# Optimization experiments

Hardware: AMD Instinct MI355X
Metric: run time of the kernel (lower is better)

Reference implementation:

```python
import jax, jax.numpy as jnp
import numpy as np

CH_N = 12
CH_N_CONST = 4
CH_E = 8
MAX_V = 100.0
DT = 1.0


def _build_graph(n_inputs, n_hid, n_actions):
    n_nodes = n_inputs + n_hid + n_actions + 1
    mid = np.arange(n_inputs, n_inputs + n_hid + n_actions)
    src = np.concatenate([
        np.repeat(np.arange(n_inputs), n_hid + n_actions),
        np.repeat(np.arange(n_inputs, n_inputs + n_hid), n_hid + n_actions),
        np.full(n_nodes - 1, n_nodes - 1),
    ])
    tgt = np.concatenate([
        np.tile(mid, n_inputs),
        np.tile(mid, n_hid),
        np.arange(n_nodes - 1),
    ])
    return src.astype(np.int32), tgt.astype(np.int32), n_nodes


def setup_inputs() -> dict:
    n_inputs, n_hid, n_actions, B = 64, 1024, 16, 2
    src, tgt, n_nodes = _build_graph(n_inputs, n_hid, n_actions)
    n_edges = src.shape[0]
    key = jax.random.key(0)
    ks = jax.random.split(key, 10)
    s = 0.05
    d_msg_in = 2 + 2 * CH_N + CH_E          # 34
    d_msg_out = 2 * (CH_N - CH_N_CONST) + CH_E  # 24
    d_upd_in = 3 * CH_N - 2 * CH_N_CONST    # 28
    return {
        "nodes": jax.random.normal(ks[0], (B, n_nodes, CH_N), jnp.float32) * s,
        "edges": jax.random.normal(ks[1], (B, n_edges, CH_E), jnp.float32) * s,
        "msg_w1": jax.random.normal(ks[2], (32, d_msg_in), jnp.float32) * s,
        "msg_b1": jax.random.normal(ks[3], (32,), jnp.float32) * s,
        "msg_w2": jax.random.normal(ks[4], (d_msg_out, 32), jnp.float32) * s,
        "msg_b2": jax.random.normal(ks[5], (d_msg_out,), jnp.float32) * s,
        "upd_w1": jax.random.normal(ks[6], (16, d_upd_in), jnp.float32) * s,
        "upd_b1": jax.random.normal(ks[7], (16,), jnp.float32) * s,
        "upd_w2": jax.random.normal(ks[8], (CH_N - CH_N_CONST, 16), jnp.float32) * s,
        "upd_b2": jax.random.normal(ks[9], (CH_N - CH_N_CONST,), jnp.float32) * s,
        "sources": jnp.asarray(src),
        "targets": jnp.asarray(tgt),
    }


def reference(nodes, edges, msg_w1, msg_b1, msg_w2, msg_b2,
              upd_w1, upd_b1, upd_w2, upd_b2, sources, targets):
    B, N, _ = nodes.shape
    E = edges.shape[1]
    d = CH_N - CH_N_CONST  # dynamic node channels = 8

    # degree features (float for concat)
    out_degs = jax.ops.segment_sum(jnp.ones((E,), nodes.dtype), sources, num_segments=N)
    in_degs = jax.ops.segment_sum(jnp.ones((E,), nodes.dtype), targets, num_segments=N)
    od = jnp.broadcast_to(out_degs[sources][None, :, None], (B, E, 1))
    idg = jnp.broadcast_to(in_degs[targets][None, :, None], (B, E, 1))

    # gather + message MLP: [B, E, 34] -> 32 -> 24
    m_x = jnp.concatenate([nodes[:, sources], nodes[:, targets], edges, od, idg], axis=2)
    h = jax.nn.relu(jnp.einsum('bef,hf->beh', m_x, msg_w1) + msg_b1)
    m = jnp.einsum('beh,oh->beo', h, msg_w2) + msg_b2
    m_a, m_b, m_ab = m[..., :d], m[..., d:2 * d], m[..., 2 * d:]

    # scatter-aggregate (mean)
    agg_a = jnp.zeros((B, N, d), m.dtype).at[:, sources].add(m_a)
    agg_b = jnp.zeros((B, N, d), m.dtype).at[:, targets].add(m_b)
    agg_a = agg_a / jnp.maximum(out_degs, 1.0)[None, :, None]
    agg_b = agg_b / jnp.maximum(in_degs, 1.0)[None, :, None]

    # update MLP: [B, N, 28] -> 16 -> 8
    u_x = jnp.concatenate([agg_a, agg_b, nodes], axis=2)
    uh = jax.nn.relu(jnp.einsum('bnf,hf->bnh', u_x, upd_w1) + upd_b1)
    update = jnp.einsum('bnh,oh->bno', uh, upd_w2) + upd_b2

    # node step (decay=0, set_nodes=False, hard clamp)
    new_dyn = jnp.clip(nodes[..., :d] + update * DT, -MAX_V, MAX_V)
    new_nodes = jnp.concatenate([new_dyn, nodes[..., d:]], axis=-1)
    # edge step (ch_e_const=0, hard clamp)
    new_edges = jnp.clip(edges + m_ab * DT, -MAX_V, MAX_V)
    return new_nodes, new_edges
```

## Files before the change

### kernel.cpp

```cpp
#include <hip/hip_runtime.h>
#include <stdint.h>

#define D_IN1 34
#define H1    32
#define D_OUT1 24
#define D_IN2 28
#define H2    16
#define D_OUT2 8
#define CHN   12
#define CHE   8

__device__ __forceinline__ float clip100(float f) { return fminf(fmaxf(f, -100.f), 100.f); }

__global__ void k_zero(int* __restrict__ p, int n_words) {
    int i = blockIdx.x * blockDim.x + threadIdx.x;
    if (i < n_words) p[i] = 0;
}

__global__ void k_degs(const int* __restrict__ src, const int* __restrict__ tgt,
                       int* __restrict__ outd, int* __restrict__ ind, int E, int N) {
    extern __shared__ int hist[];
    int* ho = hist;
    int* hi = hist + N;
    for (int k = threadIdx.x; k < 2 * N; k += blockDim.x) hist[k] = 0;
    __syncthreads();
    for (int e = blockIdx.x * blockDim.x + threadIdx.x; e < E;
         e += gridDim.x * blockDim.x) {
        int s = src[e];
        int t = tgt[e];
        int s0 = __shfl(s, 0);
        unsigned long long act = __ballot(1);
        if (__all(s == s0)) {
            if ((threadIdx.x & 63) == 0) atomicAdd(&ho[s0], (int)__popcll(act));
        } else {
            atomicAdd(&ho[s], 1);
        }
        atomicAdd(&hi[t], 1);
    }
    __syncthreads();
    for (int k = threadIdx.x; k < N; k += blockDim.x) {
        int a = ho[k], b = hi[k];
        if (a) atomicAdd(&outd[k], a);
        if (b) atomicAdd(&ind[k], b);
    }
}

__launch_bounds__(256)
__global__ void k_edge(const float* __restrict__ nodes, const float* __restrict__ edges,
                       const float* __restrict__ w1, const float* __restrict__ b1,
                       const float* __restrict__ w2, const float* __restrict__ b2,
                       const int* __restrict__ src, const int* __restrict__ tgt,
                       const int* __restrict__ outd, const int* __restrict__ ind,
                       float* __restrict__ agg_a, float* __restrict__ partials,
                       float* __restrict__ new_edges, int E, int N, int chunk, int nblk_alloc) {
    extern __shared__ float aggB[];
    int blk = blockIdx.x, b = blockIdx.y;
    int start = blk * chunk;
    if (start >= E) return;
    int end = min(E, start + chunk);

    for (int k = threadIdx.x; k < 8 * N; k += 256) aggB[k] = 0.f;
    __syncthreads();

    for (int base = start; base < end; base += 256) {
        int e = base + threadIdx.x;
        bool v = e < end;

        int s = -1, t = -1;
        float m[D_OUT1];

        if (v) {
            s = src[e];
            t = tgt[e];

            float x[D_IN1];
            const float4* ns = (const float4*)(nodes + ((size_t)b * N + s) * CHN);
            const float4* nt = (const float4*)(nodes + ((size_t)b * N + t) * CHN);
#pragma unroll
            for (int i = 0; i < 3; ++i) {
                float4 a = ns[i];
                x[4*i] = a.x; x[4*i+1] = a.y; x[4*i+2] = a.z; x[4*i+3] = a.w;
            }
#pragma unroll
            for (int i = 0; i < 3; ++i) {
                float4 a = nt[i];
                x[12+4*i] = a.x; x[13+4*i] = a.y; x[14+4*i] = a.z; x[15+4*i] = a.w;
            }
            const float4* ep = (const float4*)(edges + ((size_t)b * E + e) * CHE);
            float4 e0 = ep[0], e1 = ep[1];
            x[24] = e0.x; x[25] = e0.y; x[26] = e0.z; x[27] = e0.w;
            x[28] = e1.x; x[29] = e1.y; x[30] = e1.z; x[31] = e1.w;
            x[32] = (float)outd[s];
            x[33] = (float)ind[t];

            float hb[H1];
#pragma unroll
            for (int h = 0; h < H1; ++h) {
                float a = b1[h];
#pragma unroll
                for (int i = 0; i < D_IN1; ++i) a = fmaf(w1[h * D_IN1 + i], x[i], a);
                hb[h] = fmaxf(a, 0.f);
            }
#pragma unroll
            for (int o = 0; o < D_OUT1; ++o) {
                float a = b2[o];
#pragma unroll
                for (int j = 0; j < H1; ++j) a = fmaf(w2[o * H1 + j], hb[j], a);
                m[o] = a;
            }

            float4 o0, o1;
            o0.x = clip100(e0.x + m[16]); o0.y = clip100(e0.y + m[17]);
            o0.z = clip100(e0.z + m[18]); o0.w = clip100(e0.w + m[19]);
            o1.x = clip100(e1.x + m[20]); o1.y = clip100(e1.y + m[21]);
            o1.z = clip100(e1.z + m[22]); o1.w = clip100(e1.w + m[23]);
            float4* ow = (float4*)(new_edges + ((size_t)b * E + e) * CHE);
            ow[0] = o0; ow[1] = o1;

#pragma unroll
            for (int c = 0; c < 8; ++c) atomicAdd(&aggB[c * N + t], m[8 + c]);
        }

        int s0 = __shfl(s, 0);
        bool fast = __all(v && s == s0);
        if (fast) {
            float* ga = agg_a + ((size_t)b * N + s0) * 8;
#pragma unroll
            for (int c = 0; c < 8; ++c) {
                float vv = m[c];
#pragma unroll
                for (int off = 32; off; off >>= 1) vv += __shfl_xor(vv, off);
                if ((threadIdx.x & 63) == 0) atomicAdd(&ga[c], vv);
            }
        } else if (v) {
            float* ga = agg_a + ((size_t)b * N + s) * 8;
#pragma unroll
            for (int c = 0; c < 8; ++c) atomicAdd(&ga[c], m[c]);
        }
    }

    __syncthreads();
    float* P = partials + ((size_t)b * nblk_alloc + blk) * 8 * N;
    for (int k = threadIdx.x; k < 8 * N; k += 256) P[k] = aggB[k];
}

__global__ void k_aggb(const float* __restrict__ partials, float* __restrict__ agg_b,
                       int nblk_used, int nblk_alloc, int span, int N, int totb) {
    int id = blockIdx.x * blockDim.x + threadIdx.x;
    if (id >= totb) return;
    int p0 = blockIdx.y * span;
    int p1 = min(nblk_used, p0 + span);
    if (p0 >= p1) return;
    int b = id / (8 * N);
    int r = id % (8 * N);
    float sum = 0.f;
    for (int p = p0; p < p1; ++p)
        sum += partials[((size_t)b * nblk_alloc + p) * 8 * N + r];
    atomicAdd(&agg_b[(size_t)b * 8 * N + r], sum);
}

__launch_bounds__(256)
__global__ void k_upd(const float* __restrict__ nodes,
                      const float* __restrict__ agg_a, const float* __restrict__ agg_b,
                      const int* __restrict__ outd, const int* __restrict__ ind,
                      const float* __restrict__ u1, const float* __restrict__ ub1,
                      const float* __restrict__ u2, const float* __restrict__ ub2,
                      float* __restrict__ new_nodes, int N, int total) {
    int i = blockIdx.x * blockDim.x + threadIdx.x;
    if (i >= total) return;
    int b = i / N;
    int n = i % N;

    float rod = 1.f / fmaxf((float)outd[n], 1.f);
    float rdg = 1.f / fmaxf((float)ind[n], 1.f);

    float ux[D_IN2];
    const float4* ga = (const float4*)(agg_a + (size_t)i * 8);
    float4 a0 = ga[0], a1 = ga[1];
    ux[0] = a0.x * rod; ux[1] = a0.y * rod; ux[2] = a0.z * rod; ux[3] = a0.w * rod;
    ux[4] = a1.x * rod; ux[5] = a1.y * rod; ux[6] = a1.z * rod; ux[7] = a1.w * rod;
    const float* gb = agg_b + (size_t)b * 8 * N + n;
#pragma unroll
    for (int c = 0; c < 8; ++c) ux[8 + c] = gb[(size_t)c * N] * rdg;

    const float4* np4 = (const float4*)(nodes + (size_t)i * CHN);
    float4 n0 = np4[0], n1 = np4[1], n2 = np4[2];
    ux[16] = n0.x; ux[17] = n0.y; ux[18] = n0.z; ux[19] = n0.w;
    ux[20] = n1.x; ux[21] = n1.y; ux[22] = n1.z; ux[23] = n1.w;
    ux[24] = n2.x; ux[25] = n2.y; ux[26] = n2.z; ux[27] = n2.w;

    float hb[H2];
#pragma unroll
    for (int h = 0; h < H2; ++h) {
        float a = ub1[h];
#pragma unroll
        for (int k = 0; k < D_IN2; ++k) a = fmaf(u1[h * D_IN2 + k], ux[k], a);
        hb[h] = fmaxf(a, 0.f);
    }
    float up[D_OUT2];
#pragma unroll
    for (int o = 0; o < D_OUT2; ++o) {
        float a = ub2[o];
#pragma unroll
        for (int k = 0; k < H2; ++k) a = fmaf(u2[o * H2 + k], hb[k], a);
        up[o] = clip100(ux[16 + o] + a);
    }
    float4* onp = (float4*)(new_nodes + (size_t)i * CHN);
    onp[0] = make_float4(up[0], up[1], up[2], up[3]);
    onp[1] = make_float4(up[4], up[5], up[6], up[7]);
    onp[2] = n2;
}

extern "C" void kernel_launch(void* const* d_in, const int* in_sizes, int n_in,
                              void* d_out, int out_size, void* d_ws, size_t ws_size,
                              hipStream_t stream) {
    const float* nodes = (const float*)d_in[0];
    const float* edges = (const float*)d_in[1];
    const float* mw1   = (const float*)d_in[2];
    const float* mb1   = (const float*)d_in[3];
    const float* mw2   = (const float*)d_in[4];
    const float* mb2   = (const float*)d_in[5];
    const float* uw1   = (const float*)d_in[6];
    const float* ubb1  = (const float*)d_in[7];
    const float* uw2   = (const float*)d_in[8];
    const float* ubb2  = (const float*)d_in[9];
    const int* src     = (const int*)d_in[10];
    const int* tgt     = (const int*)d_in[11];

    int E = in_sizes[10];
    int B = in_sizes[1] / (E * 8);
    int N = in_sizes[0] / (B * 12);

    size_t off = 0;
    int* outd = (int*)((char*)d_ws + off);       off += (size_t)N * 4;
    int* ind  = (int*)((char*)d_ws + off);       off += (size_t)N * 4;
    off = (off + 63) & ~(size_t)63;
    float* agg_a = (float*)((char*)d_ws + off);  off += (size_t)B * N * 8 * 4;
    float* agg_b = (float*)((char*)d_ws + off);  off += (size_t)B * N * 8 * 4;
    size_t zbytes = off;
    off = (off + 63) & ~(size_t)63;
    float* partials = (float*)((char*)d_ws + off);

    size_t per_blk = (size_t)B * 8 * N * sizeof(float);
    size_t avail = (ws_size > off) ? (ws_size - off) : 0;
    int nblk = (int)(avail / per_blk);
    if (nblk > 512) nblk = 512;
    if (nblk < 8)   nblk = 8;

    int zwords = (int)(zbytes / 4);
    k_zero<<<(zwords + 255) / 256, 256, 0, stream>>>((int*)d_ws, zwords);

    k_degs<<<128, 256, 2 * N * sizeof(int), stream>>>(src, tgt, outd, ind, E, N);

    float* out_nodes = (float*)d_out;
    float* out_edges = out_nodes + (size_t)B * N * 12;

    int chunk = (E + nblk - 1) / nblk;
    chunk = (chunk + 255) & ~255;
    int nblk_used = (E + chunk - 1) / chunk;

    dim3 ge(nblk_used, B);
    k_edge<<<ge, 256, 8 * N * sizeof(float), stream>>>(
        nodes, edges, mw1, mb1, mw2, mb2, src, tgt, outd, ind,
        agg_a, partials, out_edges, E, N, chunk, nblk);

    int totb = B * 8 * N;
    const int P = 8;
    int span = (nblk_used + P - 1) / P;
    dim3 ga((totb + 255) / 256, P);
    k_aggb<<<ga, 256, 0, stream>>>(partials, agg_b, nblk_used, nblk, span, N, totb);

    k_upd<<<(B * N + 255) / 256, 256, 0, stream>>>(nodes, agg_a, agg_b, outd, ind,
                                                   uw1, ubb1, uw2, ubb2,
                                                   out_nodes, N, B * N);
}
```

Measured before the change: 404.5 us.

## Precompute per-node first-layer partial sums and reuse them in the edge MLP

Splits the first message-MLP layer by linearity: a new per-node kernel computes the source-node and target-node contributions (including degree terms and bias) once into SA/TB tables. The edge kernel then gathers two 32-float rows and adds only the 8 edge-feature terms, which removes most of the per-edge FMAs and the node/degree gathers. It also streams the agg_b outputs straight into shared atomics, and enlarges edge blocks to 512 threads, along with the degs grid and agg-reduction split. The cost is extra workspace and 256 bytes of gathered data per edge instead of 96.

```diff
diff --git a/kernel.cpp b/kernel.cpp
--- a/kernel.cpp
+++ b/kernel.cpp
@@ -46,11 +46,46 @@
 }
 
 __launch_bounds__(256)
-__global__ void k_edge(const float* __restrict__ nodes, const float* __restrict__ edges,
-                       const float* __restrict__ w1, const float* __restrict__ b1,
-                       const float* __restrict__ w2, const float* __restrict__ b2,
+__global__ void k_pre(const float* __restrict__ nodes,
+                      const int* __restrict__ outd, const int* __restrict__ ind,
+                      const float* __restrict__ w1, const float* __restrict__ b1,
+                      float* __restrict__ SA, float* __restrict__ TB,
+                      int N, int total) {
+    int i = blockIdx.x * blockDim.x + threadIdx.x;
+    if (i >= total) return;
+    int n = i % N;
+
+    float x[12];
+    const float4* np = (const float4*)(nodes + (size_t)i * CHN);
+    float4 n0 = np[0], n1 = np[1], n2 = np[2];
+    x[0]=n0.x; x[1]=n0.y; x[2]=n0.z; x[3]=n0.w;
+    x[4]=n1.x; x[5]=n1.y; x[6]=n1.z; x[7]=n1.w;
+    x[8]=n2.x; x[9]=n2.y; x[10]=n2.z; x[11]=n2.w;
+    float od  = (float)outd[n];
+    float idg = (float)ind[n];
+
+    float* sap = SA + (size_t)i * H1;
+    float* tbp = TB + (size_t)i * H1;
+#pragma unroll
+    for (int h = 0; h < H1; ++h) {
+        const float* wr = w1 + h * D_IN1;
+        float a = wr[32] * od;
+#pragma unroll
+        for (int k = 0; k < 12; ++k) a = fmaf(wr[k], x[k], a);
+        sap[h] = a;
+        float c = fmaf(wr[33], idg, b1[h]);
+#pragma unroll
+        for (int k = 0; k < 12; ++k) c = fmaf(wr[12 + k], x[k], c);
+        tbp[h] = c;
+    }
+}
+
+__launch_bounds__(512, 8)
+__global__ void k_edge(const float* __restrict__ edges,
+                       const float* __restrict__ SA, const float* __restrict__ TB,
+                       const float* __restrict__ w1, const float* __restrict__ w2,
+                       const float* __restrict__ b2,
                        const int* __restrict__ src, const int* __restrict__ tgt,
-                       const int* __restrict__ outd, const int* __restrict__ ind,
                        float* __restrict__ agg_a, float* __restrict__ partials,
                        float* __restrict__ new_edges, int E, int N, int chunk, int nblk_alloc) {
     extern __shared__ float aggB[];
@@ -59,66 +94,73 @@
     if (start >= E) return;
     int end = min(E, start + chunk);
 
-    for (int k = threadIdx.x; k < 8 * N; k += 256) aggB[k] = 0.f;
+    for (int k = threadIdx.x; k < 8 * N; k += 512) aggB[k] = 0.f;
     __syncthreads();
 
-    for (int base = start; base < end; base += 256) {
+    for (int base = start; base < end; base += 512) {
         int e = base + threadIdx.x;
         bool v = e < end;
 
         int s = -1, t = -1;
-        float m[D_OUT1];
+        float ma[8];
+        float4 e0, e1;
 
         if (v) {
             s = src[e];
             t = tgt[e];
 
-            float x[D_IN1];
-            const float4* ns = (const float4*)(nodes + ((size_t)b * N + s) * CHN);
-            const float4* nt = (const float4*)(nodes + ((size_t)b * N + t) * CHN);
-#pragma unroll
-            for (int i = 0; i < 3; ++i) {
-                float4 a = ns[i];
-                x[4*i] = a.x; x[4*i+1] = a.y; x[4*i+2] = a.z; x[4*i+3] = a.w;
-            }
-#pragma unroll
-            for (int i = 0; i < 3; ++i) {
-                float4 a = nt[i];
-                x[12+4*i] = a.x; x[13+4*i] = a.y; x[14+4*i] = a.z; x[15+4*i] = a.w;
-            }
             const float4* ep = (const float4*)(edges + ((size_t)b * E + e) * CHE);
-            float4 e0 = ep[0], e1 = ep[1];
-            x[24] = e0.x; x[25] = e0.y; x[26] = e0.z; x[27] = e0.w;
-            x[28] = e1.x; x[29] = e1.y; x[30] = e1.z; x[31] = e1.w;
-            x[32] = (float)outd[s];
-            x[33] = (float)ind[t];
-
-            float hb[H1];
-#pragma unroll
-            for (int h = 0; h < H1; ++h) {
-                float a = b1[h];
-#pragma unroll
-                for (int i = 0; i < D_IN1; ++i) a = fmaf(w1[h * D_IN1 + i], x[i], a);
-                hb[h] = fmaxf(a, 0.f);
-            }
-#pragma unroll
-            for (int o = 0; o < D_OUT1; ++o) {
+            e0 = ep[0]; e1 = ep[1];
+
+            const float4* sap = (const float4*)(SA + ((size_t)b * N + s) * H1);
+            const float4* tbp = (const float4*)(TB + ((size_t)b * N + t) * H1);
+
+            float h[H1];
+#pragma unroll
+            for (int q = 0; q < 8; ++q) {
+                float4 a4 = sap[q];
+                float4 c4 = tbp[q];
+                float hv[4] = { a4.x + c4.x, a4.y + c4.y, a4.z + c4.z, a4.w + c4.w };
+#pragma unroll
+                for (int r = 0; r < 4; ++r) {
+                    const float* wr = w1 + (4 * q + r) * D_IN1 + 24;
+                    float a = hv[r];
+                    a = fmaf(wr[0], e0.x, a); a = fmaf(wr[1], e0.y, a);
+                    a = fmaf(wr[2], e0.z, a); a = fmaf(wr[3], e0.w, a);
+                    a = fmaf(wr[4], e1.x, a); a = fmaf(wr[5], e1.y, a);
+                    a = fmaf(wr[6], e1.z, a); a = fmaf(wr[7], e1.w, a);
+                    h[4 * q + r] = fmaxf(a, 0.f);
+                }
+            }
+
+#pragma unroll
+            for (int o = 0; o < 8; ++o) {
                 float a = b2[o];
 #pragma unroll
-                for (int j = 0; j < H1; ++j) a = fmaf(w2[o * H1 + j], hb[j], a);
-                m[o] = a;
-            }
-
-            float4 o0, o1;
-            o0.x = clip100(e0.x + m[16]); o0.y = clip100(e0.y + m[17]);
-            o0.z = clip100(e0.z + m[18]); o0.w = clip100(e0.w + m[19]);
-            o1.x = clip100(e1.x + m[20]); o1.y = clip100(e1.y + m[21]);
-            o1.z = clip100(e1.z + m[22]); o1.w = clip100(e1.w + m[23]);
+                for (int j = 0; j < H1; ++j) a = fmaf(w2[o * H1 + j], h[j], a);
+                ma[o] = a;
+            }
+#pragma unroll
+            for (int o = 0; o < 8; ++o) {
+                float a = b2[8 + o];
+#pragma unroll
+                for (int j = 0; j < H1; ++j) a = fmaf(w2[(8 + o) * H1 + j], h[j], a);
+                atomicAdd(&aggB[o * N + t], a);
+            }
+            float mab[8];
+#pragma unroll
+            for (int o = 0; o < 8; ++o) {
+                float a = b2[16 + o];
+#pragma unroll
+                for (int j = 0; j < H1; ++j) a = fmaf(w2[(16 + o) * H1 + j], h[j], a);
+                mab[o] = a;
+            }
+            e0.x = clip100(e0.x + mab[0]); e0.y = clip100(e0.y + mab[1]);
+            e0.z = clip100(e0.z + mab[2]); e0.w = clip100(e0.w + mab[3]);
+            e1.x = clip100(e1.x + mab[4]); e1.y = clip100(e1.y + mab[5]);
+            e1.z = clip100(e1.z + mab[6]); e1.w = clip100(e1.w + mab[7]);
             float4* ow = (float4*)(new_edges + ((size_t)b * E + e) * CHE);
-            ow[0] = o0; ow[1] = o1;
-
-#pragma unroll
-            for (int c = 0; c < 8; ++c) atomicAdd(&aggB[c * N + t], m[8 + c]);
+            ow[0] = e0; ow[1] = e1;
         }
 
         int s0 = __shfl(s, 0);
@@ -127,7 +169,7 @@
             float* ga = agg_a + ((size_t)b * N + s0) * 8;
 #pragma unroll
             for (int c = 0; c < 8; ++c) {
-                float vv = m[c];
+                float vv = ma[c];
 #pragma unroll
                 for (int off = 32; off; off >>= 1) vv += __shfl_xor(vv, off);
                 if ((threadIdx.x & 63) == 0) atomicAdd(&ga[c], vv);
@@ -135,13 +177,13 @@
         } else if (v) {
             float* ga = agg_a + ((size_t)b * N + s) * 8;
 #pragma unroll
-            for (int c = 0; c < 8; ++c) atomicAdd(&ga[c], m[c]);
+            for (int c = 0; c < 8; ++c) atomicAdd(&ga[c], ma[c]);
         }
     }
 
     __syncthreads();
     float* P = partials + ((size_t)b * nblk_alloc + blk) * 8 * N;
-    for (int k = threadIdx.x; k < 8 * N; k += 256) P[k] = aggB[k];
+    for (int k = threadIdx.x; k < 8 * N; k += 512) P[k] = aggB[k];
 }
 
 __global__ void k_aggb(const float* __restrict__ partials, float* __restrict__ agg_b,
@@ -238,6 +280,8 @@
     float* agg_a = (float*)((char*)d_ws + off);  off += (size_t)B * N * 8 * 4;
     float* agg_b = (float*)((char*)d_ws + off);  off += (size_t)B * N * 8 * 4;
     size_t zbytes = off;
+    float* SA = (float*)((char*)d_ws + off);     off += (size_t)B * N * H1 * 4;
+    float* TB = (float*)((char*)d_ws + off);     off += (size_t)B * N * H1 * 4;
     off = (off + 63) & ~(size_t)63;
     float* partials = (float*)((char*)d_ws + off);
 
@@ -250,27 +294,31 @@
     int zwords = (int)(zbytes / 4);
     k_zero<<<(zwords + 255) / 256, 256, 0, stream>>>((int*)d_ws, zwords);
 
-    k_degs<<<128, 256, 2 * N * sizeof(int), stream>>>(src, tgt, outd, ind, E, N);
+    k_degs<<<256, 256, 2 * N * sizeof(int), stream>>>(src, tgt, outd, ind, E, N);
+
+    int totn = B * N;
+    k_pre<<<(totn + 255) / 256, 256, 0, stream>>>(nodes, outd, ind, mw1, mb1,
+                                                  SA, TB, N, totn);
 
     float* out_nodes = (float*)d_out;
     float* out_edges = out_nodes + (size_t)B * N * 12;
 
     int chunk = (E + nblk - 1) / nblk;
-    chunk = (chunk + 255) & ~255;
+    chunk = (chunk + 511) & ~511;
     int nblk_used = (E + chunk - 1) / chunk;
 
     dim3 ge(nblk_used, B);
-    k_edge<<<ge, 256, 8 * N * sizeof(float), stream>>>(
-        nodes, edges, mw1, mb1, mw2, mb2, src, tgt, outd, ind,
+    k_edge<<<ge, 512, 8 * N * sizeof(float), stream>>>(
+        edges, SA, TB, mw1, mw2, mb2, src, tgt,
         agg_a, partials, out_edges, E, N, chunk, nblk);
 
     int totb = B * 8 * N;
-    const int P = 8;
+    const int P = 16;
     int span = (nblk_used + P - 1) / P;
     dim3 ga((totb + 255) / 256, P);
     k_aggb<<<ga, 256, 0, stream>>>(partials, agg_b, nblk_used, nblk, span, N, totb);
 
-    k_upd<<<(B * N + 255) / 256, 256, 0, stream>>>(nodes, agg_a, agg_b, outd, ind,
-                                                   uw1, ubb1, uw2, ubb2,
-                                                   out_nodes, N, B * N);
-}
+    k_upd<<<(totn + 255) / 256, 256, 0, stream>>>(nodes, agg_a, agg_b, outd, ind,
+                                                  uw1, ubb1, uw2, ubb2,
+                                                  out_nodes, N, totn);
+}
```

Result: slower. 848.7 us (+109.8%).
